# Kernel tuning notes

Measured on AMD Instinct MI355X. Metric: run time of the kernel, lower is better.

The kernel has to match this reference:

```python
import jax, jax.numpy as jnp
import numpy as np

N_NODES = 200000  # graph size
D = 128           # feature dim == out_size
N1 = 81920        # layer-1 node set size
B = 8192          # batch size
K = 10            # num_sample neighbors


def setup_inputs() -> dict:
    key = jax.random.key(0)
    k = jax.random.split(key, 7)
    raw_features = jax.random.normal(k[0], (N_NODES, D), dtype=jnp.float32)
    # xavier-like scale for weights [out, 2*in]
    W1 = jax.random.normal(k[1], (D, 2 * D), dtype=jnp.float32) * (1.0 / np.sqrt(2 * D))
    W2 = jax.random.normal(k[2], (D, 2 * D), dtype=jnp.float32) * (1.0 / np.sqrt(2 * D))
    layer1_nodes = jax.random.randint(k[3], (N1,), 0, N_NODES)
    neigh0_idx = jax.random.randint(k[4], (N1, K), 0, N_NODES)
    map_batch = jax.random.randint(k[5], (B,), 0, N1)
    neigh1_idx = jax.random.randint(k[6], (B, K), 0, N1)
    return {
        "raw_features": raw_features,
        "W1": W1,
        "W2": W2,
        "layer1_nodes": layer1_nodes,
        "neigh0_idx": neigh0_idx,
        "map_batch": map_batch,
        "neigh1_idx": neigh1_idx,
    }


def _sage_layer(self_feats, agg_feats, W):
    # combined = cat([self, agg], dim=1); relu(W @ combined.T).T == relu(combined @ W.T)
    combined = jnp.concatenate([self_feats, agg_feats], axis=1)
    return jax.nn.relu(combined @ W.T)


def reference(raw_features, W1, W2, layer1_nodes, neigh0_idx, map_batch, neigh1_idx):
    # Layer 1: aggregate raw features over K sampled neighbors (MEAN), gcn=False
    agg0 = jnp.mean(raw_features[neigh0_idx], axis=1)        # [N1, D]
    self0 = raw_features[layer1_nodes]                        # [N1, D]
    h1 = _sage_layer(self0, agg0, W1)                         # [N1, D]
    # Layer 2: aggregate layer-1 embeddings for the batch nodes
    agg1 = jnp.mean(h1[neigh1_idx], axis=1)                   # [B, D]
    self1 = h1[map_batch]                                     # [B, D]
    h2 = _sage_layer(self1, agg1, W2)                         # [B, D]
    return h2
```

## Files before the change

### kernel.cpp

```cpp
#include <hip/hip_runtime.h>
#include <stdint.h>

#define D 128
#define K_NEI 10
#define TILE_M 64

typedef __bf16 bf16x8 __attribute__((ext_vector_type(8)));
typedef float f32x4 __attribute__((ext_vector_type(4)));

__device__ __forceinline__ uint32_t f2bf(float f) {
    union { float f; uint32_t u; } v; v.f = f;
    uint32_t u = v.u;
    return (u + 0x7FFFu + ((u >> 16) & 1u)) >> 16;
}
__device__ __forceinline__ float bf2f(uint32_t h) {
    union { uint32_t u; float f; } v; v.u = h << 16; return v.f;
}
__device__ __forceinline__ uint32_t pack2(float a, float b) {
    return f2bf(a) | (f2bf(b) << 16);
}

template <bool FEATS_F32, bool OUT_F32>
__global__ void sage_layer(const void* __restrict__ feats_,
                           const float* __restrict__ W,
                           const int* __restrict__ self_idx,
                           const int* __restrict__ neigh_idx,
                           void* __restrict__ out_)
{
    __shared__ __align__(16) uint16_t Alds[TILE_M * 128];
    __shared__ __align__(16) uint16_t Wlds[128 * 128];

    const int tid  = threadIdx.x;
    const int wave = tid >> 6;
    const int lane = tid & 63;
    const int r16  = lane & 15;
    const int q    = lane >> 4;
    const int G    = blockIdx.x * TILE_M;

    const float*    feats_f = (const float*)feats_;
    const uint16_t* feats_b = (const uint16_t*)feats_;

    f32x4 acc[8];
    #pragma unroll
    for (int nt = 0; nt < 8; ++nt) acc[nt] = (f32x4){0.f, 0.f, 0.f, 0.f};

    for (int half = 0; half < 2; ++half) {
        #pragma unroll
        for (int it = 0; it < 8; ++it) {
            int t = it * 256 + tid;
            int j = t >> 4, c = t & 15;
            const float* src = W + (size_t)j * 256 + half * 128 + c * 8;
            f32x4 w0 = *(const f32x4*)(src);
            f32x4 w1 = *(const f32x4*)(src + 4);
            uint4 o;
            o.x = pack2(w0[0], w0[1]); o.y = pack2(w0[2], w0[3]);
            o.z = pack2(w1[0], w1[1]); o.w = pack2(w1[2], w1[3]);
            int cs = c ^ (j & 15);
            *(uint4*)(Wlds + j * 128 + cs * 8) = o;
        }
        if (half == 0) {
            #pragma unroll
            for (int it = 0; it < 4; ++it) {
                int t = it * 256 + tid;
                int n = t >> 4, c = t & 15;
                int node = self_idx[G + n];
                uint4 o;
                if (FEATS_F32) {
                    const float* src = feats_f + (size_t)node * D + c * 8;
                    f32x4 f0 = *(const f32x4*)(src);
                    f32x4 f1 = *(const f32x4*)(src + 4);
                    o.x = pack2(f0[0], f0[1]); o.y = pack2(f0[2], f0[3]);
                    o.z = pack2(f1[0], f1[1]); o.w = pack2(f1[2], f1[3]);
                } else {
                    o = *(const uint4*)(feats_b + (size_t)node * D + c * 8);
                }
                int cs = c ^ (n & 15);
                *(uint4*)(Alds + n * 128 + cs * 8) = o;
            }
        } else {
            #pragma unroll
            for (int it = 0; it < 4; ++it) {
                int t = it * 256 + tid;
                int n = t >> 4, c = t & 15;
                const int* nrow = neigh_idx + (size_t)(G + n) * K_NEI;
                float s0=0,s1=0,s2=0,s3=0,s4=0,s5=0,s6=0,s7=0;
                #pragma unroll
                for (int k = 0; k < K_NEI; ++k) {
                    if (FEATS_F32) {
                        const float* src = feats_f + (size_t)nrow[k] * D + c * 8;
                        f32x4 f0 = *(const f32x4*)(src);
                        f32x4 f1 = *(const f32x4*)(src + 4);
                        s0 += f0[0]; s1 += f0[1]; s2 += f0[2]; s3 += f0[3];
                        s4 += f1[0]; s5 += f1[1]; s6 += f1[2]; s7 += f1[3];
                    } else {
                        uint4 v = *(const uint4*)(feats_b + (size_t)nrow[k] * D + c * 8);
                        s0 += bf2f(v.x & 0xFFFFu); s1 += bf2f(v.x >> 16);
                        s2 += bf2f(v.y & 0xFFFFu); s3 += bf2f(v.y >> 16);
                        s4 += bf2f(v.z & 0xFFFFu); s5 += bf2f(v.z >> 16);
                        s6 += bf2f(v.w & 0xFFFFu); s7 += bf2f(v.w >> 16);
                    }
                }
                const float inv = 0.1f;
                uint4 o;
                o.x = pack2(s0 * inv, s1 * inv);
                o.y = pack2(s2 * inv, s3 * inv);
                o.z = pack2(s4 * inv, s5 * inv);
                o.w = pack2(s6 * inv, s7 * inv);
                int cs = c ^ (n & 15);
                *(uint4*)(Alds + n * 128 + cs * 8) = o;
            }
        }
        __syncthreads();

        #pragma unroll
        for (int ks = 0; ks < 4; ++ks) {
            int cidx = ks * 4 + q;
            bf16x8 a = *(const bf16x8*)(Alds + (wave * 16 + r16) * 128 + ((cidx ^ r16) * 8));
            bf16x8 b[8];
            #pragma unroll
            for (int nt = 0; nt < 8; ++nt) {
                int j = nt * 16 + r16;
                b[nt] = *(const bf16x8*)(Wlds + j * 128 + ((cidx ^ r16) * 8));
            }
            #pragma unroll
            for (int nt = 0; nt < 8; ++nt)
                acc[nt] = __builtin_amdgcn_mfma_f32_16x16x32_bf16(a, b[nt], acc[nt], 0, 0, 0);
        }
        __syncthreads();
    }

    const int row_base = G + wave * 16 + q * 4;
    #pragma unroll
    for (int nt = 0; nt < 8; ++nt) {
        int col = nt * 16 + r16;
        #pragma unroll
        for (int r = 0; r < 4; ++r) {
            float v = acc[nt][r];
            v = v > 0.f ? v : 0.f;
            if (OUT_F32) ((float*)out_)[(size_t)(row_base + r) * D + col] = v;
            else ((uint16_t*)out_)[(size_t)(row_base + r) * D + col] = (uint16_t)f2bf(v);
        }
    }
}

__global__ void probe(float* p) { *p = 12345.0f; }

extern "C" void kernel_launch(void* const* d_in, const int* in_sizes, int n_in,
                              void* d_out, int out_size, void* d_ws, size_t ws_size,
                              hipStream_t stream) {
    const float* raw = (const float*)d_in[0];
    const float* W1  = (const float*)d_in[1];
    const float* W2  = (const float*)d_in[2];
    const int* layer1_nodes = (const int*)d_in[3];
    const int* neigh0       = (const int*)d_in[4];
    const int* map_batch    = (const int*)d_in[5];
    const int* neigh1       = (const int*)d_in[6];

    uint16_t* h1 = (uint16_t*)d_ws;

    const int N1 = in_sizes[3];
    const int B  = in_sizes[5];

    probe<<<1, 1, 0, stream>>>((float*)d_out + (out_size - 1));
    sage_layer<true,  false><<<N1 / TILE_M, 256, 0, stream>>>(raw, W1, layer1_nodes, neigh0, h1);
    sage_layer<false, true ><<<B  / TILE_M, 256, 0, stream>>>(h1,  W2, map_batch,    neigh1, d_out);
}
```

Before: 251.8 us.

## Split gather/aggregate into separate kernel and stage concatenated A through workspace

Each layer is split into two kernels. A build_A kernel gathers self features and averages neighbor features into a bf16 concatenated matrix in global workspace, and a separate gemm_relu kernel loads tiles of that matrix and runs the MFMA GEMM. The aim is to give the latency-bound random gathers a high-occupancy kernel without the large LDS footprint, so they no longer stall the GEMM blocks. The cost is an extra global write and read of the A matrix and two more launches. It also drops the probe kernel, and falls back to the fused path if the workspace is too small.

```diff
diff --git a/kernel.cpp b/kernel.cpp
--- a/kernel.cpp
+++ b/kernel.cpp
@@ -18,6 +18,140 @@
 }
 __device__ __forceinline__ uint32_t pack2(float a, float b) {
     return f2bf(a) | (f2bf(b) << 16);
+}
+
+template <bool FEATS_F32>
+__global__ void build_A(const void* __restrict__ feats_,
+                        const int* __restrict__ self_idx,
+                        const int* __restrict__ neigh_idx,
+                        uint16_t* __restrict__ A, int M)
+{
+    const int t = blockIdx.x * 256 + threadIdx.x;
+    const int i = t >> 4;
+    const int j = t & 15;
+    if (i >= M) return;
+
+    const float*    ff = (const float*)feats_;
+    const uint16_t* fb = (const uint16_t*)feats_;
+
+    {
+        int node = self_idx[i];
+        uint4 o;
+        if (FEATS_F32) {
+            const float* src = ff + (size_t)node * D + j * 8;
+            f32x4 a = *(const f32x4*)src;
+            f32x4 b = *(const f32x4*)(src + 4);
+            o.x = pack2(a[0], a[1]); o.y = pack2(a[2], a[3]);
+            o.z = pack2(b[0], b[1]); o.w = pack2(b[2], b[3]);
+        } else {
+            o = *(const uint4*)(fb + (size_t)node * D + j * 8);
+        }
+        *(uint4*)(A + (size_t)i * 256 + j * 8) = o;
+    }
+
+    const int* nrow = neigh_idx + (size_t)i * K_NEI;
+    int idx[K_NEI];
+    #pragma unroll
+    for (int k = 0; k < K_NEI; ++k) idx[k] = nrow[k];
+
+    float s0=0,s1=0,s2=0,s3=0,s4=0,s5=0,s6=0,s7=0;
+    #pragma unroll
+    for (int k = 0; k < K_NEI; ++k) {
+        if (FEATS_F32) {
+            const float* src = ff + (size_t)idx[k] * D + j * 8;
+            f32x4 a = *(const f32x4*)src;
+            f32x4 b = *(const f32x4*)(src + 4);
+            s0 += a[0]; s1 += a[1]; s2 += a[2]; s3 += a[3];
+            s4 += b[0]; s5 += b[1]; s6 += b[2]; s7 += b[3];
+        } else {
+            uint4 v = *(const uint4*)(fb + (size_t)idx[k] * D + j * 8);
+            s0 += bf2f(v.x & 0xFFFFu); s1 += bf2f(v.x >> 16);
+            s2 += bf2f(v.y & 0xFFFFu); s3 += bf2f(v.y >> 16);
+            s4 += bf2f(v.z & 0xFFFFu); s5 += bf2f(v.z >> 16);
+            s6 += bf2f(v.w & 0xFFFFu); s7 += bf2f(v.w >> 16);
+        }
+    }
+    const float inv = 0.1f;
+    uint4 o;
+    o.x = pack2(s0 * inv, s1 * inv);
+    o.y = pack2(s2 * inv, s3 * inv);
+    o.z = pack2(s4 * inv, s5 * inv);
+    o.w = pack2(s6 * inv, s7 * inv);
+    *(uint4*)(A + (size_t)i * 256 + 128 + j * 8) = o;
+}
+
+template <bool OUT_F32>
+__global__ void gemm_relu(const uint16_t* __restrict__ A,
+                          const float* __restrict__ W,
+                          void* __restrict__ out_)
+{
+    __shared__ __align__(16) uint16_t Alds[TILE_M * 128];
+    __shared__ __align__(16) uint16_t Wlds[128 * 128];
+
+    const int tid  = threadIdx.x;
+    const int wave = tid >> 6;
+    const int lane = tid & 63;
+    const int r16  = lane & 15;
+    const int q    = lane >> 4;
+    const int G    = blockIdx.x * TILE_M;
+
+    f32x4 acc[8];
+    #pragma unroll
+    for (int nt = 0; nt < 8; ++nt) acc[nt] = (f32x4){0.f, 0.f, 0.f, 0.f};
+
+    for (int half = 0; half < 2; ++half) {
+        #pragma unroll
+        for (int it = 0; it < 8; ++it) {
+            int t = it * 256 + tid;
+            int j = t >> 4, c = t & 15;
+            const float* src = W + (size_t)j * 256 + half * 128 + c * 8;
+            f32x4 w0 = *(const f32x4*)(src);
+            f32x4 w1 = *(const f32x4*)(src + 4);
+            uint4 o;
+            o.x = pack2(w0[0], w0[1]); o.y = pack2(w0[2], w0[3]);
+            o.z = pack2(w1[0], w1[1]); o.w = pack2(w1[2], w1[3]);
+            int cs = c ^ (j & 15);
+            *(uint4*)(Wlds + j * 128 + cs * 8) = o;
+        }
+        #pragma unroll
+        for (int it = 0; it < 4; ++it) {
+            int t = it * 256 + tid;
+            int n = t >> 4, c = t & 15;
+            uint4 v = *(const uint4*)(A + (size_t)(G + n) * 256 + half * 128 + c * 8);
+            int cs = c ^ (n & 15);
+            *(uint4*)(Alds + n * 128 + cs * 8) = v;
+        }
+        __syncthreads();
+
+        #pragma unroll
+        for (int ks = 0; ks < 4; ++ks) {
+            int cidx = ks * 4 + q;
+            bf16x8 a = *(const bf16x8*)(Alds + (wave * 16 + r16) * 128 + ((cidx ^ r16) * 8));
+            bf16x8 b[8];
+            #pragma unroll
+            for (int nt = 0; nt < 8; ++nt) {
+                int jj = nt * 16 + r16;
+                b[nt] = *(const bf16x8*)(Wlds + jj * 128 + ((cidx ^ r16) * 8));
+            }
+            #pragma unroll
+            for (int nt = 0; nt < 8; ++nt)
+                acc[nt] = __builtin_amdgcn_mfma_f32_16x16x32_bf16(a, b[nt], acc[nt], 0, 0, 0);
+        }
+        __syncthreads();
+    }
+
+    const int row_base = G + wave * 16 + q * 4;
+    #pragma unroll
+    for (int nt = 0; nt < 8; ++nt) {
+        int col = nt * 16 + r16;
+        #pragma unroll
+        for (int r = 0; r < 4; ++r) {
+            float v = acc[nt][r];
+            v = v > 0.f ? v : 0.f;
+            if (OUT_F32) ((float*)out_)[(size_t)(row_base + r) * D + col] = v;
+            else ((uint16_t*)out_)[(size_t)(row_base + r) * D + col] = (uint16_t)f2bf(v);
+        }
+    }
 }
 
 template <bool FEATS_F32, bool OUT_F32>
@@ -119,8 +253,8 @@
             bf16x8 b[8];
             #pragma unroll
             for (int nt = 0; nt < 8; ++nt) {
-                int j = nt * 16 + r16;
-                b[nt] = *(const bf16x8*)(Wlds + j * 128 + ((cidx ^ r16) * 8));
+                int jj = nt * 16 + r16;
+                b[nt] = *(const bf16x8*)(Wlds + jj * 128 + ((cidx ^ r16) * 8));
             }
             #pragma unroll
             for (int nt = 0; nt < 8; ++nt)
@@ -142,8 +276,6 @@
         }
     }
 }
-
-__global__ void probe(float* p) { *p = 12345.0f; }
 
 extern "C" void kernel_launch(void* const* d_in, const int* in_sizes, int n_in,
                               void* d_out, int out_size, void* d_ws, size_t ws_size,
@@ -156,12 +288,23 @@
     const int* map_batch    = (const int*)d_in[5];
     const int* neigh1       = (const int*)d_in[6];
 
-    uint16_t* h1 = (uint16_t*)d_ws;
-
     const int N1 = in_sizes[3];
     const int B  = in_sizes[5];
 
-    probe<<<1, 1, 0, stream>>>((float*)d_out + (out_size - 1));
-    sage_layer<true,  false><<<N1 / TILE_M, 256, 0, stream>>>(raw, W1, layer1_nodes, neigh0, h1);
-    sage_layer<false, true ><<<B  / TILE_M, 256, 0, stream>>>(h1,  W2, map_batch,    neigh1, d_out);
-}
+    const size_t needed = (size_t)N1 * 256 * 2 + (size_t)N1 * 128 * 2 + (size_t)B * 256 * 2;
+
+    if (ws_size >= needed) {
+        uint16_t* A1 = (uint16_t*)d_ws;
+        uint16_t* h1 = A1 + (size_t)N1 * 256;
+        uint16_t* A2 = h1 + (size_t)N1 * 128;
+
+        build_A<true ><<<(N1 * 16 + 255) / 256, 256, 0, stream>>>(raw, layer1_nodes, neigh0, A1, N1);
+        gemm_relu<false><<<N1 / TILE_M, 256, 0, stream>>>(A1, W1, h1);
+        build_A<false><<<(B * 16 + 255) / 256, 256, 0, stream>>>(h1, map_batch, neigh1, A2, B);
+        gemm_relu<true ><<<B / TILE_M, 256, 0, stream>>>(A2, W2, d_out);
+    } else {
+        uint16_t* h1 = (uint16_t*)d_ws;
+        sage_layer<true,  false><<<N1 / TILE_M, 256, 0, stream>>>(raw, W1, layer1_nodes, neigh0, h1);
+        sage_layer<false, true ><<<B  / TILE_M, 256, 0, stream>>>(h1,  W2, map_batch,    neigh1, d_out);
+    }
+}
```

Result: faster. 246.6 us (-2.1%).
